# Kernel optimization log

Hardware: AMD Instinct MI355X
Metric: run time of the kernel (lower is better)

The kernel has to match this reference:

```python
import jax, jax.numpy as jnp
import numpy as np

N = 100000   # nodes
E = 3200000  # edges (avg degree 32)
G = 64       # graphs in batch
IN_DIM, HID, NCLS = 260, 128, 16


def setup_inputs() -> dict:
    key = jax.random.key(0)
    ks = jax.random.split(key, 14)

    def lin_w(k, fan_in, fan_out):
        return (jax.random.normal(k, (fan_in, fan_out), jnp.float32)
                / np.float32(np.sqrt(fan_in)))

    return {
        "x": jax.random.normal(ks[0], (N, IN_DIM), jnp.float32),
        "edge_index": jax.random.randint(ks[1], (2, E), 0, N, dtype=jnp.int32),
        "batch": jnp.sort(jax.random.randint(ks[2], (N,), 0, G, dtype=jnp.int32)),
        "w1": lin_w(ks[3], IN_DIM, HID), "b1": jnp.zeros((HID,), jnp.float32),
        "w2": lin_w(ks[4], HID, HID),    "b2": jnp.zeros((HID,), jnp.float32),
        "w3": lin_w(ks[5], HID, HID),    "b3": jnp.zeros((HID,), jnp.float32),
        "fc1_w": lin_w(ks[6], HID, 128), "fc1_b": jnp.zeros((128,), jnp.float32),
        "fc2_w": lin_w(ks[7], 128, NCLS),"fc2_b": jnp.zeros((NCLS,), jnp.float32),
    }


def reference(x, edge_index, batch, w1, b1, w2, b2, w3, b3,
              fc1_w, fc1_b, fc2_w, fc2_b):
    # --- GCN normalization (PyG GCNConv default: add self-loops, D^-1/2 A D^-1/2)
    loops = jnp.arange(N, dtype=edge_index.dtype)
    src = jnp.concatenate([edge_index[0], loops])  # [E+N]
    dst = jnp.concatenate([edge_index[1], loops])  # [E+N]
    deg = jax.ops.segment_sum(jnp.ones_like(dst, jnp.float32), dst,
                              num_segments=N)      # in-degree incl. self-loop
    dinv = jnp.where(deg > 0, jax.lax.rsqrt(deg), 0.0)
    norm = (dinv[src] * dinv[dst])[:, None]        # [E+N, 1]

    def gcn_conv(h, w, b):
        h = h @ w                                  # dense transform first
        msg = h[src] * norm                        # gather + scale  [E+N, HID]
        out = jax.ops.segment_sum(msg, dst, num_segments=N)  # scatter-add
        return out + b

    h = jax.nn.relu(gcn_conv(x, w1, b1))
    h = jax.nn.relu(gcn_conv(h, w2, b2))
    h = jax.nn.relu(gcn_conv(h, w3, b3))

    # --- global mean pool over graph ids
    sums = jax.ops.segment_sum(h, batch, num_segments=G)                # [G, HID]
    cnts = jax.ops.segment_sum(jnp.ones((N,), jnp.float32), batch, G)   # [G]
    pooled = sums / jnp.maximum(cnts, 1.0)[:, None]

    # --- MLP head
    z = jax.nn.relu(pooled @ fc1_w + fc1_b)
    return z @ fc2_w + fc2_b                       # [G, NCLS]
```

## Files before the change

kernel.cpp:

```cpp
#include <hip/hip_runtime.h>

#define HID 128

#define NB 256
#define BW 400
#define DEPTH 24
#define CH 2048

typedef __attribute__((ext_vector_type(8))) short bf16x8;
typedef __attribute__((ext_vector_type(4))) float f32x4;

__device__ inline float blo(unsigned u) { return __uint_as_float(u << 16); }
__device__ inline float bhi(unsigned u) { return __uint_as_float(u & 0xffff0000u); }
__device__ inline unsigned rne16(float x) {
  unsigned u = __float_as_uint(x);
  return (u + 0x7fffu + ((u >> 16) & 1u)) >> 16;
}
__device__ inline unsigned pk2(float a, float b) { return (rne16(b) << 16) | rne16(a); }

__device__ inline void prep_one(const float* __restrict__ W, unsigned* __restrict__ Wt,
                                int K, int KP2, int b) {
  int idx = b * 256 + threadIdx.x;
  if (idx >= 128 * KP2) return;
  int c = idx / KP2, kk = idx - c * KP2;
  int k0 = kk * 2, k1 = k0 + 1;
  float v0 = (k0 < K) ? W[(long)k0 * 128 + c] : 0.f;
  float v1 = (k1 < K) ? W[(long)k1 * 128 + c] : 0.f;
  Wt[idx] = pk2(v0, v1);
}

__global__ void k_prep_init(const float* __restrict__ w1, const float* __restrict__ w2,
                            const float* __restrict__ w3, unsigned* __restrict__ Wt1,
                            unsigned* __restrict__ Wt2, unsigned* __restrict__ Wt3,
                            float* __restrict__ psum, int* __restrict__ gstart,
                            int* __restrict__ bhist, int IN, int G) {
  int b = blockIdx.x;
  if (b < 72) prep_one(w1, Wt1, IN, 144, b);
  else if (b < 104) prep_one(w2, Wt2, 128, 64, b - 72);
  else prep_one(w3, Wt3, 128, 64, b - 104);
  if (b < 32) {
    int i = b * 256 + threadIdx.x;
    if (i < G * HID) psum[i] = 0.f;
    if (i <= G) gstart[i] = -1;
    if (i < NB) bhist[i] = 0;
  }
}

__global__ __launch_bounds__(256) void k_hist(const int* __restrict__ dst, int E, int N,
                                              int* __restrict__ bhist) {
  __shared__ int h[NB];
  int t = threadIdx.x;
  h[t] = 0;
  __syncthreads();
  int i = blockIdx.x * blockDim.x + t;
  int stride = gridDim.x * blockDim.x;
  for (; i < E; i += stride) {
    int b = (int)(((long long)dst[i] * NB) / N);
    atomicAdd(&h[b], 1);
  }
  __syncthreads();
  if (h[t]) atomicAdd(&bhist[t], h[t]);
}

__global__ __launch_bounds__(NB) void k_bscan(const int* __restrict__ bhist,
                                              int* __restrict__ bstart,
                                              int* __restrict__ gcur, int E) {
  __shared__ int sh[NB];
  int t = threadIdx.x;
  int v = bhist[t];
  sh[t] = v;
  __syncthreads();
  for (int off = 1; off < NB; off <<= 1) {
    int x = (t >= off) ? sh[t - off] : 0;
    __syncthreads();
    sh[t] += x;
    __syncthreads();
  }
  int excl = sh[t] - v;
  bstart[t] = excl;
  gcur[t] = excl;
  if (t == NB - 1) bstart[NB] = sh[t];
}

__global__ __launch_bounds__(256) void k_scatter(const int* __restrict__ src,
                                                 const int* __restrict__ dst,
                                                 int E, int N,
                                                 unsigned* __restrict__ binned,
                                                 int* __restrict__ gcur) {
  __shared__ unsigned buf[NB][DEPTH];
  __shared__ int cnt[NB];
  int t = threadIdx.x;
  long cover = (long)gridDim.x * CH;
  int nround = (int)((E + cover - 1) / cover);
  for (int r = 0; r < nround; ++r) {
    cnt[t] = 0;
    __syncthreads();
    long base = (long)r * cover + (long)blockIdx.x * CH;
#pragma unroll
    for (int k = 0; k < CH / 256; ++k) {
      long i = base + k * 256 + t;
      if (i < E) {
        int s = src[i], d = dst[i];
        int b = (int)(((long long)d * NB) / N);
        int d0 = (int)(((long long)b * N + NB - 1) / NB);
        unsigned pack = ((unsigned)(d - d0) << 17) | (unsigned)s;
        int slot = atomicAdd(&cnt[b], 1);
        if (slot < DEPTH) buf[b][slot] = pack;
        else { int g = atomicAdd(&gcur[b], 1); binned[g] = pack; }
      }
    }
    __syncthreads();
    {
      int c = cnt[t];
      if (c > DEPTH) c = DEPTH;
      if (c > 0) {
        int g = atomicAdd(&gcur[t], c);
        for (int k = 0; k < c; ++k) binned[g + k] = buf[t][k];
      }
    }
    __syncthreads();
  }
}

__global__ __launch_bounds__(256) void k_build(const unsigned* __restrict__ binned,
                                               const int* __restrict__ bstart, int N,
                                               int* __restrict__ deg,
                                               float* __restrict__ dinv,
                                               int* __restrict__ rowstart,
                                               int* __restrict__ csr) {
  __shared__ int hist[BW];
  __shared__ int loc[BW];
  __shared__ int scanbuf[256];
  int b = blockIdx.x;
  int t = threadIdx.x;
  int d0 = (int)(((long long)b * N + NB - 1) / NB);
  int d1 = (int)(((long long)(b + 1) * N + NB - 1) / NB);
  if (d1 > N) d1 = N;
  int W = d1 - d0;
  for (int w = t; w < BW; w += 256) hist[w] = 0;
  __syncthreads();
  int s = bstart[b], e = bstart[b + 1];
  for (int i = s + t; i < e; i += 256)
    atomicAdd(&hist[binned[i] >> 17], 1);
  __syncthreads();
  int e0 = t * 2, e1 = t * 2 + 1;
  int h0 = (e0 < W) ? hist[e0] : 0;
  int h1 = (e1 < W) ? hist[e1] : 0;
  scanbuf[t] = h0 + h1;
  __syncthreads();
  for (int off = 1; off < 256; off <<= 1) {
    int x = (t >= off) ? scanbuf[t - off] : 0;
    __syncthreads();
    scanbuf[t] += x;
    __syncthreads();
  }
  int excl = scanbuf[t] - (h0 + h1);
  if (e0 < W) loc[e0] = excl;
  if (e1 < W) loc[e1] = excl + h0;
  if (e0 < W) {
    deg[d0 + e0] = h0;
    dinv[d0 + e0] = rsqrtf((float)(h0 + 1));
    rowstart[d0 + e0] = s + loc[e0];
    hist[e0] = 0;
  }
  if (e1 < W) {
    deg[d0 + e1] = h1;
    dinv[d0 + e1] = rsqrtf((float)(h1 + 1));
    rowstart[d0 + e1] = s + loc[e1];
    hist[e1] = 0;
  }
  __syncthreads();
  for (int i = s + t; i < e; i += 256) {
    unsigned p = binned[i];
    int dl = (int)(p >> 17);
    int sn = (int)(p & 0x1ffffu);
    int pos = s + loc[dl] + atomicAdd(&hist[dl], 1);
    csr[pos] = sn;
  }
}

__global__ __launch_bounds__(256) void k_gemm_mf(const unsigned* __restrict__ A,
                                                 const unsigned* __restrict__ Wt,
                                                 const float* __restrict__ dscale,
                                                 unsigned* __restrict__ Cu, int N) {
  int t = threadIdx.x;
  int w = t >> 6;
  int l = t & 63;
  int lr = l & 15;
  int kg = l >> 4;
  int wr0 = blockIdx.x * 128 + w * 32;

  f32x4 acc[2][8];
#pragma unroll
  for (int rt = 0; rt < 2; ++rt)
#pragma unroll
    for (int f = 0; f < 8; ++f) acc[rt][f] = (f32x4){0.f, 0.f, 0.f, 0.f};

  int r0 = wr0 + lr, r1 = wr0 + 16 + lr;
#pragma unroll
  for (int kt = 0; kt < 4; ++kt) {
    int ko = kt * 16 + kg * 4;
    bf16x8 a0 = {}, a1 = {};
    if (r0 < N) a0 = *(const bf16x8*)&A[(long)r0 * 64 + ko];
    if (r1 < N) a1 = *(const bf16x8*)&A[(long)r1 * 64 + ko];
#pragma unroll
    for (int f = 0; f < 8; ++f) {
      bf16x8 b = *(const bf16x8*)&Wt[(f * 16 + lr) * 64 + ko];
      acc[0][f] = __builtin_amdgcn_mfma_f32_16x16x32_bf16(a0, b, acc[0][f], 0, 0, 0);
      acc[1][f] = __builtin_amdgcn_mfma_f32_16x16x32_bf16(a1, b, acc[1][f], 0, 0, 0);
    }
  }
#pragma unroll
  for (int rt = 0; rt < 2; ++rt) {
#pragma unroll
    for (int reg = 0; reg < 4; ++reg) {
      int row = wr0 + rt * 16 + kg * 4 + reg;
      float ds = (row < N) ? dscale[row] : 0.f;
#pragma unroll
      for (int f = 0; f < 8; ++f) {
        float v = acc[rt][f][reg] * ds;
        float pv = __shfl_xor(v, 1);
        if (!(l & 1) && row < N)
          Cu[(long)row * 64 + ((f * 16 + lr) >> 1)] = pk2(v, pv);
      }
    }
  }
}

__global__ __launch_bounds__(256) void k_gemm1_mf(const float* __restrict__ X,
                                                  const unsigned* __restrict__ Wt,
                                                  const float* __restrict__ dscale,
                                                  unsigned* __restrict__ Cu, int N, int K) {
  int t = threadIdx.x;
  int w = t >> 6;
  int l = t & 63;
  int lr = l & 15;
  int kg = l >> 4;
  int wr0 = blockIdx.x * 128 + w * 32;

  f32x4 acc[2][8];
#pragma unroll
  for (int rt = 0; rt < 2; ++rt)
#pragma unroll
    for (int f = 0; f < 8; ++f) acc[rt][f] = (f32x4){0.f, 0.f, 0.f, 0.f};

  int r0 = wr0 + lr, r1 = wr0 + 16 + lr;
  int nkt = (K + 31) / 32;
  for (int kt = 0; kt < nkt; ++kt) {
    int kb = kt * 32 + kg * 8;
    bf16x8 a0 = {}, a1 = {};
    if (kb + 7 < K) {
      if (r0 < N) {
        const float* p = &X[(long)r0 * K + kb];
        float4 u = *(const float4*)p, v = *(const float4*)(p + 4);
        union { uint4 q; bf16x8 b; } cv;
        cv.q.x = pk2(u.x, u.y); cv.q.y = pk2(u.z, u.w);
        cv.q.z = pk2(v.x, v.y); cv.q.w = pk2(v.z, v.w);
        a0 = cv.b;
      }
      if (r1 < N) {
        const float* p = &X[(long)r1 * K + kb];
        float4 u = *(const float4*)p, v = *(const float4*)(p + 4);
        union { uint4 q; bf16x8 b; } cv;
        cv.q.x = pk2(u.x, u.y); cv.q.y = pk2(u.z, u.w);
        cv.q.z = pk2(v.x, v.y); cv.q.w = pk2(v.z, v.w);
        a1 = cv.b;
      }
    } else if (kb < K) {
      float t0[8], t1[8];
#pragma unroll
      for (int j = 0; j < 8; ++j) {
        int k = kb + j;
        t0[j] = (r0 < N && k < K) ? X[(long)r0 * K + k] : 0.f;
        t1[j] = (r1 < N && k < K) ? X[(long)r1 * K + k] : 0.f;
      }
      union { uint4 q; bf16x8 b; } c0, c1;
      c0.q.x = pk2(t0[0], t0[1]); c0.q.y = pk2(t0[2], t0[3]);
      c0.q.z = pk2(t0[4], t0[5]); c0.q.w = pk2(t0[6], t0[7]);
      c1.q.x = pk2(t1[0], t1[1]); c1.q.y = pk2(t1[2], t1[3]);
      c1.q.z = pk2(t1[4], t1[5]); c1.q.w = pk2(t1[6], t1[7]);
      a0 = c0.b; a1 = c1.b;
    }
    int ko = kt * 16 + kg * 4;
#pragma unroll
    for (int f = 0; f < 8; ++f) {
      bf16x8 b = *(const bf16x8*)&Wt[(f * 16 + lr) * 144 + ko];
      acc[0][f] = __builtin_amdgcn_mfma_f32_16x16x32_bf16(a0, b, acc[0][f], 0, 0, 0);
      acc[1][f] = __builtin_amdgcn_mfma_f32_16x16x32_bf16(a1, b, acc[1][f], 0, 0, 0);
    }
  }
#pragma unroll
  for (int rt = 0; rt < 2; ++rt) {
#pragma unroll
    for (int reg = 0; reg < 4; ++reg) {
      int row = wr0 + rt * 16 + kg * 4 + reg;
      float ds = (row < N) ? dscale[row] : 0.f;
#pragma unroll
      for (int f = 0; f < 8; ++f) {
        float v = acc[rt][f][reg] * ds;
        float pv = __shfl_xor(v, 1);
        if (!(l & 1) && row < N)
          Cu[(long)row * 64 + ((f * 16 + lr) >> 1)] = pk2(v, pv);
      }
    }
  }
}

__global__ __launch_bounds__(256) void k_agg(const uint4* __restrict__ T4,
                                             const float* __restrict__ dinv,
                                             const int* __restrict__ rowstart,
                                             const int* __restrict__ deg,
                                             const int* __restrict__ csr,
                                             const float* __restrict__ bias,
                                             uint4* __restrict__ outu,
                                             int N) {
  int t = threadIdx.x;
  int grp = t >> 4;
  int lane = t & 15;
  int i = blockIdx.x * 16 + grp;
  if (i >= N) return;

  int c0 = lane * 8;
  float b0 = bias[c0 + 0], b1 = bias[c0 + 1], b2 = bias[c0 + 2], b3 = bias[c0 + 3];
  float b4 = bias[c0 + 4], b5 = bias[c0 + 5], b6 = bias[c0 + 6], b7 = bias[c0 + 7];

  uint4 su = T4[(long)i * 16 + lane];
  float a0 = blo(su.x), a1 = bhi(su.x), a2 = blo(su.y), a3 = bhi(su.y);
  float a4 = blo(su.z), a5 = bhi(su.z), a6 = blo(su.w), a7 = bhi(su.w);

  int s0 = rowstart[i];
  int d = deg[i];
  int j = 0;
  for (; j + 3 < d; j += 4) {
    int n1 = csr[s0 + j];
    int n2 = csr[s0 + j + 1];
    int n3 = csr[s0 + j + 2];
    int n4 = csr[s0 + j + 3];
    uint4 u1 = T4[(long)n1 * 16 + lane];
    uint4 u2 = T4[(long)n2 * 16 + lane];
    uint4 u3 = T4[(long)n3 * 16 + lane];
    uint4 u4 = T4[(long)n4 * 16 + lane];
    a0 += (blo(u1.x) + blo(u2.x)) + (blo(u3.x) + blo(u4.x));
    a1 += (bhi(u1.x) + bhi(u2.x)) + (bhi(u3.x) + bhi(u4.x));
    a2 += (blo(u1.y) + blo(u2.y)) + (blo(u3.y) + blo(u4.y));
    a3 += (bhi(u1.y) + bhi(u2.y)) + (bhi(u3.y) + bhi(u4.y));
    a4 += (blo(u1.z) + blo(u2.z)) + (blo(u3.z) + blo(u4.z));
    a5 += (bhi(u1.z) + bhi(u2.z)) + (bhi(u3.z) + bhi(u4.z));
    a6 += (blo(u1.w) + blo(u2.w)) + (blo(u3.w) + blo(u4.w));
    a7 += (bhi(u1.w) + bhi(u2.w)) + (bhi(u3.w) + bhi(u4.w));
  }
  for (; j < d; ++j) {
    int n1 = csr[s0 + j];
    uint4 u1 = T4[(long)n1 * 16 + lane];
    a0 += blo(u1.x); a1 += bhi(u1.x); a2 += blo(u1.y); a3 += bhi(u1.y);
    a4 += blo(u1.z); a5 += bhi(u1.z); a6 += blo(u1.w); a7 += bhi(u1.w);
  }
  float di = dinv[i];
  float v0 = fmaxf(di * a0 + b0, 0.f);
  float v1 = fmaxf(di * a1 + b1, 0.f);
  float v2 = fmaxf(di * a2 + b2, 0.f);
  float v3 = fmaxf(di * a3 + b3, 0.f);
  float v4 = fmaxf(di * a4 + b4, 0.f);
  float v5 = fmaxf(di * a5 + b5, 0.f);
  float v6 = fmaxf(di * a6 + b6, 0.f);
  float v7 = fmaxf(di * a7 + b7, 0.f);
  uint4 o;
  o.x = pk2(v0, v1); o.y = pk2(v2, v3); o.z = pk2(v4, v5); o.w = pk2(v6, v7);
  outu[(long)i * 16 + lane] = o;
}

__global__ void k_starts(const int* __restrict__ batch, int N, int* __restrict__ start) {
  int i = blockIdx.x * blockDim.x + threadIdx.x;
  int stride = gridDim.x * blockDim.x;
  for (; i < N; i += stride) {
    int g = batch[i];
    if (i == 0) {
      start[g] = 0;
    } else if (batch[i - 1] != g) {
      start[g] = i;
    }
  }
}

__global__ __launch_bounds__(256) void k_fix_starts(int* __restrict__ start, int G, int N) {
  __shared__ int sh[256];
  int t = threadIdx.x;
  int v = (t < G) ? start[t] : N;
  if (v < 0) v = N;
  sh[t] = v;
  __syncthreads();
  for (int off = 1; off < 256; off <<= 1) {
    int x = (t + off < 256) ? sh[t + off] : N;
    int nv = min(sh[t], x);
    __syncthreads();
    sh[t] = nv;
    __syncthreads();
  }
  if (t < G) start[t] = sh[t];
  if (t == 0) start[G] = N;
}

__global__ __launch_bounds__(256) void k_pool2(const unsigned* __restrict__ hu,
                                               const int* __restrict__ batch,
                                               float* __restrict__ psum, int N) {
  int t = threadIdx.x;
  int rg = t >> 6;
  int lane = t & 63;
  long base = (long)blockIdx.x * 64;
  float a0 = 0.f, a1 = 0.f;
  int cur = -1;
#pragma unroll
  for (int j = 0; j < 16; ++j) {
    long r = base + j * 4 + rg;
    if (r >= N) break;
    int g = batch[r];
    if (g != cur) {
      if (cur >= 0) {
        atomicAdd(&psum[cur * HID + lane * 2], a0);
        atomicAdd(&psum[cur * HID + lane * 2 + 1], a1);
        a0 = 0.f; a1 = 0.f;
      }
      cur = g;
    }
    unsigned u = hu[r * 64 + lane];
    a0 += blo(u); a1 += bhi(u);
  }
  if (cur >= 0) {
    atomicAdd(&psum[cur * HID + lane * 2], a0);
    atomicAdd(&psum[cur * HID + lane * 2 + 1], a1);
  }
}

__global__ __launch_bounds__(128) void k_head(const float* __restrict__ psum,
                                              const int* __restrict__ gstart,
                                              const float* __restrict__ fc1w,
                                              const float* __restrict__ fc1b,
                                              const float* __restrict__ fc2w,
                                              const float* __restrict__ fc2b,
                                              float* __restrict__ out, int G) {
  __shared__ float pooled[HID];
  __shared__ float z1[HID];
  int g = blockIdx.x;
  int c = threadIdx.x;
  float cn = fmaxf((float)(gstart[g + 1] - gstart[g]), 1.f);
  pooled[c] = psum[g * HID + c] / cn;
  __syncthreads();
  float a = fc1b[c];
#pragma unroll 8
  for (int k = 0; k < HID; ++k) a += pooled[k] * fc1w[k * HID + c];
  z1[c] = fmaxf(a, 0.f);
  __syncthreads();
  if (c < 16) {
    float o = fc2b[c];
#pragma unroll 8
    for (int k = 0; k < HID; ++k) o += z1[k] * fc2w[k * 16 + c];
    out[g * 16 + c] = o;
  }
}

extern "C" void kernel_launch(void* const* d_in, const int* in_sizes, int n_in,
                              void* d_out, int out_size, void* d_ws, size_t ws_size,
                              hipStream_t stream) {
  const float* x     = (const float*)d_in[0];
  const int*   ei    = (const int*)d_in[1];
  const int*   batch = (const int*)d_in[2];
  const float* w1    = (const float*)d_in[3];
  const float* b1    = (const float*)d_in[4];
  const float* w2    = (const float*)d_in[5];
  const float* b2    = (const float*)d_in[6];
  const float* w3    = (const float*)d_in[7];
  const float* b3    = (const float*)d_in[8];
  const float* fc1w  = (const float*)d_in[9];
  const float* fc1b  = (const float*)d_in[10];
  const float* fc2w  = (const float*)d_in[11];
  const float* fc2b  = (const float*)d_in[12];
  float* out = (float*)d_out;

  const int IN = in_sizes[3] / HID;
  const int N  = in_sizes[0] / IN;
  const int E  = in_sizes[1] / 2;
  const int G  = out_size / 16;

  const int* srcp = ei;
  const int* dstp = ei + E;

  char* wsp = (char*)d_ws;
  auto alloc = [&](size_t bytes) {
    char* p = wsp;
    wsp += (bytes + 255) & ~(size_t)255;
    return p;
  };
  int*   deg      = (int*)alloc((size_t)N * 4);
  int*   rowstart = (int*)alloc((size_t)N * 4);
  int*   bhist    = (int*)alloc(NB * 4);
  int*   bstart   = (int*)alloc((NB + 1) * 4);
  int*   gcur     = (int*)alloc(NB * 4);
  int*   gstart   = (int*)alloc((size_t)(G + 1) * 4);
  float* dinv     = (float*)alloc((size_t)N * 4);
  float* psum     = (float*)alloc((size_t)G * HID * 4);
  unsigned* Wt1   = (unsigned*)alloc(128 * 144 * 4);
  unsigned* Wt2   = (unsigned*)alloc(128 * 64 * 4);
  unsigned* Wt3   = (unsigned*)alloc(128 * 64 * 4);
  int*   csr      = (int*)alloc((size_t)E * 4);
  unsigned* bufA  = (unsigned*)alloc((size_t)N * 64 * 4);
  unsigned* bufB  = (unsigned*)alloc((size_t)N * 64 * 4);
  unsigned* binned = (unsigned*)bufA;

  k_prep_init<<<136, 256, 0, stream>>>(w1, w2, w3, Wt1, Wt2, Wt3,
                                       psum, gstart, bhist, IN, G);

  k_hist<<<512, 256, 0, stream>>>(dstp, E, N, bhist);
  k_bscan<<<1, NB, 0, stream>>>(bhist, bstart, gcur, E);
  k_scatter<<<782, 256, 0, stream>>>(srcp, dstp, E, N, binned, gcur);
  k_build<<<NB, 256, 0, stream>>>(binned, bstart, N, deg, dinv, rowstart, csr);

  k_starts<<<256, 256, 0, stream>>>(batch, N, gstart);
  k_fix_starts<<<1, 256, 0, stream>>>(gstart, G, N);

  int gblocks = (N + 127) / 128;
  int ablocks = (N + 15) / 16;
  k_gemm1_mf<<<gblocks, 256, 0, stream>>>(x, Wt1, dinv, bufA, N, IN);
  k_agg<<<ablocks, 256, 0, stream>>>((const uint4*)bufA, dinv, rowstart, deg, csr, b1,
                                     (uint4*)bufB, N);

  k_gemm_mf<<<gblocks, 256, 0, stream>>>(bufB, Wt2, dinv, bufA, N);
  k_agg<<<ablocks, 256, 0, stream>>>((const uint4*)bufA, dinv, rowstart, deg, csr, b2,
                                     (uint4*)bufB, N);

  k_gemm_mf<<<gblocks, 256, 0, stream>>>(bufB, Wt3, dinv, bufA, N);
  k_agg<<<ablocks, 256, 0, stream>>>((const uint4*)bufA, dinv, rowstart, deg, csr, b3,
                                     (uint4*)bufB, N);

  int pblocks = (N + 63) / 64;
  k_pool2<<<pblocks, 256, 0, stream>>>(bufB, batch, psum, N);
  k_head<<<G, 128, 0, stream>>>(psum, gstart, fc1w, fc1b, fc2w, fc2b, out, G);
}
```

Before: 580.3 us.

## Vectorize edge loads in histogram/scatter and stage GEMM1 input through LDS

The histogram and binning kernels now read dst/src with int4 loads: four edges per thread per iteration in the histogram, and eight contiguous edges per thread in the scatter, replacing strided scalar loads. The first-layer GEMM now loads X cooperatively as coalesced float4 rows into a shared-memory bf16 tile before the MFMA loop, instead of each lane doing strided 32-byte row reads. This aims to improve global memory coalescing, at the cost of two block barriers per k-tile in the GEMM. The int4 casts also assume the src/dst buffers are 16-byte aligned.

```diff
diff --git a/kernel.cpp b/kernel.cpp
--- a/kernel.cpp
+++ b/kernel.cpp
@@ -52,11 +52,20 @@
   int t = threadIdx.x;
   h[t] = 0;
   __syncthreads();
+  int E4 = E >> 2;
+  const int4* d4 = (const int4*)dst;
   int i = blockIdx.x * blockDim.x + t;
   int stride = gridDim.x * blockDim.x;
-  for (; i < E; i += stride) {
-    int b = (int)(((long long)dst[i] * NB) / N);
-    atomicAdd(&h[b], 1);
+  for (; i < E4; i += stride) {
+    int4 v = d4[i];
+    atomicAdd(&h[(int)(((long long)v.x * NB) / N)], 1);
+    atomicAdd(&h[(int)(((long long)v.y * NB) / N)], 1);
+    atomicAdd(&h[(int)(((long long)v.z * NB) / N)], 1);
+    atomicAdd(&h[(int)(((long long)v.w * NB) / N)], 1);
+  }
+  if (blockIdx.x == 0) {
+    for (int e = E4 * 4 + t; e < E; e += 256)
+      atomicAdd(&h[(int)(((long long)dst[e] * NB) / N)], 1);
   }
   __syncthreads();
   if (h[t]) atomicAdd(&bhist[t], h[t]);
@@ -95,19 +104,28 @@
   for (int r = 0; r < nround; ++r) {
     cnt[t] = 0;
     __syncthreads();
-    long base = (long)r * cover + (long)blockIdx.x * CH;
-#pragma unroll
-    for (int k = 0; k < CH / 256; ++k) {
-      long i = base + k * 256 + t;
-      if (i < E) {
-        int s = src[i], d = dst[i];
-        int b = (int)(((long long)d * NB) / N);
-        int d0 = (int)(((long long)b * N + NB - 1) / NB);
-        unsigned pack = ((unsigned)(d - d0) << 17) | (unsigned)s;
-        int slot = atomicAdd(&cnt[b], 1);
-        if (slot < DEPTH) buf[b][slot] = pack;
-        else { int g = atomicAdd(&gcur[b], 1); binned[g] = pack; }
-      }
+    long e0 = (long)r * cover + (long)blockIdx.x * CH + (long)t * 8;
+    int svals[8], dvals[8];
+    int cntv = 0;
+    if (e0 + 8 <= E) {
+      int4 s0 = *(const int4*)&src[e0], s1 = *(const int4*)&src[e0 + 4];
+      int4 d0 = *(const int4*)&dst[e0], d1 = *(const int4*)&dst[e0 + 4];
+      svals[0]=s0.x; svals[1]=s0.y; svals[2]=s0.z; svals[3]=s0.w;
+      svals[4]=s1.x; svals[5]=s1.y; svals[6]=s1.z; svals[7]=s1.w;
+      dvals[0]=d0.x; dvals[1]=d0.y; dvals[2]=d0.z; dvals[3]=d0.w;
+      dvals[4]=d1.x; dvals[5]=d1.y; dvals[6]=d1.z; dvals[7]=d1.w;
+      cntv = 8;
+    } else {
+      for (long e = e0; e < E; ++e) { svals[cntv]=src[e]; dvals[cntv]=dst[e]; ++cntv; }
+    }
+    for (int k = 0; k < cntv; ++k) {
+      int s = svals[k], d = dvals[k];
+      int b = (int)(((long long)d * NB) / N);
+      int d0b = (int)(((long long)b * N + NB - 1) / NB);
+      unsigned pack = ((unsigned)(d - d0b) << 17) | (unsigned)s;
+      int slot = atomicAdd(&cnt[b], 1);
+      if (slot < DEPTH) buf[b][slot] = pack;
+      else { int g = atomicAdd(&gcur[b], 1); binned[g] = pack; }
     }
     __syncthreads();
     {
@@ -231,12 +249,14 @@
                                                   const unsigned* __restrict__ Wt,
                                                   const float* __restrict__ dscale,
                                                   unsigned* __restrict__ Cu, int N, int K) {
+  __shared__ unsigned As[128 * 20];
   int t = threadIdx.x;
   int w = t >> 6;
   int l = t & 63;
   int lr = l & 15;
   int kg = l >> 4;
-  int wr0 = blockIdx.x * 128 + w * 32;
+  int blk0 = blockIdx.x * 128;
+  int wr0 = blk0 + w * 32;
 
   f32x4 acc[2][8];
 #pragma unroll
@@ -244,43 +264,34 @@
 #pragma unroll
     for (int f = 0; f < 8; ++f) acc[rt][f] = (f32x4){0.f, 0.f, 0.f, 0.f};
 
-  int r0 = wr0 + lr, r1 = wr0 + 16 + lr;
+  int srow = t >> 3;
+  int skq = (t & 7) * 4;
+  int rl0 = w * 32 + lr, rl1 = w * 32 + 16 + lr;
   int nkt = (K + 31) / 32;
   for (int kt = 0; kt < nkt; ++kt) {
-    int kb = kt * 32 + kg * 8;
-    bf16x8 a0 = {}, a1 = {};
-    if (kb + 7 < K) {
-      if (r0 < N) {
-        const float* p = &X[(long)r0 * K + kb];
-        float4 u = *(const float4*)p, v = *(const float4*)(p + 4);
-        union { uint4 q; bf16x8 b; } cv;
-        cv.q.x = pk2(u.x, u.y); cv.q.y = pk2(u.z, u.w);
-        cv.q.z = pk2(v.x, v.y); cv.q.w = pk2(v.z, v.w);
-        a0 = cv.b;
+    int kbase = kt * 32;
+#pragma unroll
+    for (int p = 0; p < 4; ++p) {
+      int row = p * 32 + srow;
+      int gr = blk0 + row;
+      int k = kbase + skq;
+      float4 v = make_float4(0.f, 0.f, 0.f, 0.f);
+      if (gr < N) {
+        if (k + 3 < K) {
+          v = *(const float4*)&X[(long)gr * K + k];
+        } else if (k < K) {
+          float tmp[4] = {0.f, 0.f, 0.f, 0.f};
+          for (int j = 0; j < 4; ++j)
+            if (k + j < K) tmp[j] = X[(long)gr * K + k + j];
+          v = make_float4(tmp[0], tmp[1], tmp[2], tmp[3]);
+        }
       }
-      if (r1 < N) {
-        const float* p = &X[(long)r1 * K + kb];
-        float4 u = *(const float4*)p, v = *(const float4*)(p + 4);
-        union { uint4 q; bf16x8 b; } cv;
-        cv.q.x = pk2(u.x, u.y); cv.q.y = pk2(u.z, u.w);
-        cv.q.z = pk2(v.x, v.y); cv.q.w = pk2(v.z, v.w);
-        a1 = cv.b;
-      }
-    } else if (kb < K) {
-      float t0[8], t1[8];
-#pragma unroll
-      for (int j = 0; j < 8; ++j) {
-        int k = kb + j;
-        t0[j] = (r0 < N && k < K) ? X[(long)r0 * K + k] : 0.f;
-        t1[j] = (r1 < N && k < K) ? X[(long)r1 * K + k] : 0.f;
-      }
-      union { uint4 q; bf16x8 b; } c0, c1;
-      c0.q.x = pk2(t0[0], t0[1]); c0.q.y = pk2(t0[2], t0[3]);
-      c0.q.z = pk2(t0[4], t0[5]); c0.q.w = pk2(t0[6], t0[7]);
-      c1.q.x = pk2(t1[0], t1[1]); c1.q.y = pk2(t1[2], t1[3]);
-      c1.q.z = pk2(t1[4], t1[5]); c1.q.w = pk2(t1[6], t1[7]);
-      a0 = c0.b; a1 = c1.b;
-    }
+      As[row * 20 + (skq >> 1)] = pk2(v.x, v.y);
+      As[row * 20 + (skq >> 1) + 1] = pk2(v.z, v.w);
+    }
+    __syncthreads();
+    bf16x8 a0 = *(const bf16x8*)&As[rl0 * 20 + kg * 4];
+    bf16x8 a1 = *(const bf16x8*)&As[rl1 * 20 + kg * 4];
     int ko = kt * 16 + kg * 4;
 #pragma unroll
     for (int f = 0; f < 8; ++f) {
@@ -288,6 +299,7 @@
       acc[0][f] = __builtin_amdgcn_mfma_f32_16x16x32_bf16(a0, b, acc[0][f], 0, 0, 0);
       acc[1][f] = __builtin_amdgcn_mfma_f32_16x16x32_bf16(a1, b, acc[1][f], 0, 0, 0);
     }
+    __syncthreads();
   }
 #pragma unroll
   for (int rt = 0; rt < 2; ++rt) {
```

New measurement: 604.0 us. 1.04x slower.
